# Kernel tuning notes

Measured on AMD Instinct MI355X. Metric: run time of the kernel, lower is better.

Reference implementation:

```python
import jax, jax.numpy as jnp
import numpy as np

INPUT_DIM = 512
HIDDEN_DIM = 1024
OUTPUT_DIM = 1000
BATCH = 256
SEQ_LEN = 256


def setup_inputs() -> dict:
    key = jax.random.key(0)
    ks = jax.random.split(key, 7)
    std = 1.0 / np.sqrt(HIDDEN_DIM)
    u = lambda k, shape: jax.random.uniform(k, shape, jnp.float32, -std, std)
    return {
        "x": jax.random.normal(ks[0], (BATCH, SEQ_LEN, INPUT_DIM), jnp.float32),
        "w_x2h": u(ks[1], (4 * HIDDEN_DIM, INPUT_DIM)),
        "b_x2h": u(ks[2], (4 * HIDDEN_DIM,)),
        "w_h2h": u(ks[3], (4 * HIDDEN_DIM, HIDDEN_DIM)),
        "b_h2h": u(ks[4], (4 * HIDDEN_DIM,)),
        "w_fc": u(ks[5], (OUTPUT_DIM, HIDDEN_DIM)),
        "b_fc": u(ks[6], (OUTPUT_DIM,)),
    }


def _lstm_last_hidden(x, w_x2h, b_x2h, w_h2h, b_h2h):
    B, T, D = x.shape
    H = w_h2h.shape[1]
    # Precompute input-to-hidden for all timesteps in one big GEMM: [B,T,4H]
    xg = jnp.einsum("btd,gd->btg", x, w_x2h) + b_x2h + b_h2h
    xg = jnp.swapaxes(xg, 0, 1)  # [T,B,4H] for scan

    def step(carry, xg_t):
        h, c = carry
        gates = xg_t + h @ w_h2h.T  # [B,4H]
        i, f, g, o = jnp.split(gates, 4, axis=1)
        i = jax.nn.sigmoid(i)
        f = jax.nn.sigmoid(f)
        g = jnp.tanh(g)
        o = jax.nn.sigmoid(o)
        c = c * f + i * g
        h = o * jnp.tanh(c)
        return (h, c), None

    h0 = jnp.zeros((B, H), x.dtype)
    c0 = jnp.zeros((B, H), x.dtype)
    (h_last, _), _ = jax.lax.scan(step, (h0, c0), xg)
    return h_last


def reference(x, w_x2h, b_x2h, w_h2h, b_h2h, w_fc, b_fc):
    h_last = _lstm_last_hidden(x, w_x2h, b_x2h, w_h2h, b_h2h)  # [B,H]
    return h_last @ w_fc.T + b_fc  # [B,OUTPUT_DIM]
```

## Files before the change

### kernel.cpp

```cpp
#include <hip/hip_runtime.h>

typedef __attribute__((ext_vector_type(8))) short short8;
typedef __attribute__((ext_vector_type(4))) float floatx4;

#define DIN  512
#define HSZ  1024
#define G4   4096
#define KTOT 1536
#define BQ   256
#define TT   256

#define MFMA __builtin_amdgcn_mfma_f32_16x16x32_bf16

__device__ __forceinline__ unsigned short f2bf(float f){
  unsigned int u = __float_as_uint(f);
  u += 0x7fffu + ((u >> 16) & 1u);
  return (unsigned short)(u >> 16);
}
__device__ __forceinline__ unsigned int pack2(float a, float b){
  return (unsigned int)f2bf(a) | ((unsigned int)f2bf(b) << 16);
}

__global__ void prep_wcat(const float* __restrict__ wx, const float* __restrict__ wh,
                          const float* __restrict__ bx, const float* __restrict__ bh,
                          unsigned short* __restrict__ Wcat, float* __restrict__ bias){
  int gid = blockIdx.x * blockDim.x + threadIdx.x;
  int idx = gid * 8;
  int g = idx / KTOT;
  int k = idx - g * KTOT;
  const float* src = (k < DIN) ? (wx + (size_t)g * DIN + k)
                               : (wh + (size_t)g * HSZ + (k - DIN));
  float4 f0 = *(const float4*)(src);
  float4 f1 = *(const float4*)(src + 4);
  uint4 v = make_uint4(pack2(f0.x,f0.y), pack2(f0.z,f0.w), pack2(f1.x,f1.y), pack2(f1.z,f1.w));
  *(uint4*)(Wcat + (size_t)g * KTOT + k) = v;
  if (gid < G4) bias[gid] = bx[gid] + bh[gid];
}

__global__ void prep_wfc(const float* __restrict__ wfc, unsigned short* __restrict__ Wfcb){
  int gid = blockIdx.x * blockDim.x + threadIdx.x;
  int idx = gid * 8;
  int n = idx >> 10;
  int k = idx & 1023;
  uint4 v;
  if (n < 1000){
    const float* src = wfc + (size_t)n * 1024 + k;
    float4 f0 = *(const float4*)(src);
    float4 f1 = *(const float4*)(src + 4);
    v = make_uint4(pack2(f0.x,f0.y), pack2(f0.z,f0.w), pack2(f1.x,f1.y), pack2(f1.z,f1.w));
  } else {
    v = make_uint4(0u, 0u, 0u, 0u);
  }
  *(uint4*)(Wfcb + idx) = v;
}

__global__ void prep_x(const float* __restrict__ x, unsigned short* __restrict__ xbf){
  int gid = blockIdx.x * 256 + threadIdx.x;
  int d8 = gid & 63;
  int b  = (gid >> 6) & 255;
  int t  = gid >> 14;
  const float* src = x + (((size_t)b * TT) + t) * DIN + d8 * 8;
  float4 f0 = *(const float4*)(src);
  float4 f1 = *(const float4*)(src + 4);
  uint4 v = make_uint4(pack2(f0.x,f0.y), pack2(f0.z,f0.w), pack2(f1.x,f1.y), pack2(f1.z,f1.w));
  *(uint4*)(xbf + (((size_t)t * BQ) + b) * DIN + d8 * 8) = v;
}

__global__ void init_misc(unsigned int* __restrict__ h0w, unsigned int* __restrict__ flags, int nflags){
  int gid = blockIdx.x * 256 + threadIdx.x;
  if (gid < 131072) h0w[gid] = 0u;
  if (gid < nflags) flags[gid] = 0u;
}

__global__ __launch_bounds__(512, 2)
void lstm_persist(const unsigned short* __restrict__ xbf,
                  const unsigned short* __restrict__ Wcat,
                  const float* __restrict__ bias,
                  unsigned short* __restrict__ hseq,
                  unsigned int* __restrict__ flags){
  extern __shared__ char smem[];
  char*  Ws  = smem;
  float* Gt2 = (float*)(smem + 98304);
  float* Bls = (float*)(smem + 98304 + 34816);
  __shared__ int mbx;

  const int tid  = threadIdx.x;
  const int bx   = blockIdx.x;
  const int bg   = bx >> 7;
  const int b0   = bg << 7;
  const int hb   = bx & 127;
  const int u0   = hb << 3;
  const int lane = tid & 63;
  const int w    = tid >> 6;
  const int kg   = w & 1;
  const int rg   = w >> 1;

  {
    int c  = tid >> 4;
    int ch = tid & 15;
    int grow = (c >> 3) * HSZ + u0 + (c & 7);
    const char* src = (const char*)(Wcat + (size_t)grow * KTOT);
    char* dst = Ws + c * 3072;
    int xr = (c & 7) << 4;
    #pragma unroll
    for (int q = 0; q < 12; ++q){
      int k2 = ch * 192 + q * 16;
      *(uint4*)(dst + (k2 ^ xr)) = *(const uint4*)(src + k2);
    }
    if (tid < 32) Bls[tid] = bias[(size_t)(tid >> 3) * HSZ + u0 + (tid & 7)];
    if (tid == 0) mbx = 0;
  }
  __syncthreads();

  const int kq8 = (lane >> 4) * 8;
  const int cA  = lane & 15;
  const int cB  = 16 + (lane & 15);
  const char* bpA = Ws + cA * 3072; const int xorA = (cA & 7) << 4;
  const char* bpB = Ws + cB * 3072; const int xorB = (cB & 7) << 4;

  const size_t rowA0 = (size_t)(b0 + rg * 32 + (lane & 15));

  const int er = tid >> 2;
  const int up = (tid & 3) * 2;
  float cst0 = 0.f, cst1 = 0.f;

  floatx4 xacc[2][2];

  auto compute_x = [&](int t){
    const unsigned short* xr0p = xbf + ((size_t)t * BQ + rowA0) * DIN + kg * 256 + kq8;
    const unsigned short* xr1p = xr0p + 16 * DIN;
    short8 X0[8], X1[8];
    #pragma unroll
    for (int p = 0; p < 8; ++p){
      X0[p] = *(const short8*)(xr0p + p * 32);
      X1[p] = *(const short8*)(xr1p + p * 32);
    }
    __builtin_amdgcn_sched_barrier(0);
    #pragma unroll
    for (int rf = 0; rf < 2; ++rf)
      #pragma unroll
      for (int cf = 0; cf < 2; ++cf)
        xacc[rf][cf] = (floatx4){0.f,0.f,0.f,0.f};
    const int bbase = kg * 512 + kq8 * 2;
    short8 bA[2], bB[2];
    bA[0] = *(const short8*)(bpA + ((bbase     ) ^ xorA));
    bB[0] = *(const short8*)(bpB + ((bbase     ) ^ xorB));
    bA[1] = *(const short8*)(bpA + ((bbase + 64) ^ xorA));
    bB[1] = *(const short8*)(bpB + ((bbase + 64) ^ xorB));
    #pragma unroll
    for (int j = 0; j < 8; ++j){
      const int sl = j & 1;
      short8 b0v = bA[sl], b1v = bB[sl];
      if (j < 6){
        int bb = bbase + (j + 2) * 64;
        bA[sl] = *(const short8*)(bpA + (bb ^ xorA));
        bB[sl] = *(const short8*)(bpB + (bb ^ xorB));
      }
      xacc[0][0] = MFMA(X0[j], b0v, xacc[0][0], 0, 0, 0);
      xacc[0][1] = MFMA(X0[j], b1v, xacc[0][1], 0, 0, 0);
      xacc[1][0] = MFMA(X1[j], b0v, xacc[1][0], 0, 0, 0);
      xacc[1][1] = MFMA(X1[j], b1v, xacc[1][1], 0, 0, 0);
    }
  };

  compute_x(0);

  const unsigned int* fz = flags + (bg << 7);

  for (int t = 0; t < TT; ++t){
    const unsigned short* hin  = hseq + (size_t)t * (BQ * HSZ);
    unsigned short*       hout = hseq + (size_t)(t + 1) * (BQ * HSZ);

    if (t > 0){
      if (w == 0){
        while (true){
          unsigned int va = __hip_atomic_load(fz + lane,      __ATOMIC_RELAXED, __HIP_MEMORY_SCOPE_AGENT);
          unsigned int vb = __hip_atomic_load(fz + 64 + lane, __ATOMIC_RELAXED, __HIP_MEMORY_SCOPE_AGENT);
          if (__ballot(va >= (unsigned)t && vb >= (unsigned)t) == ~0ull) break;
          __builtin_amdgcn_s_sleep(1);
        }
        if (lane == 0)
          __hip_atomic_store(&mbx, t, __ATOMIC_RELAXED, __HIP_MEMORY_SCOPE_WORKGROUP);
      } else {
        while (__hip_atomic_load(&mbx, __ATOMIC_RELAXED, __HIP_MEMORY_SCOPE_WORKGROUP) < t)
          __builtin_amdgcn_s_sleep(1);
      }
      asm volatile("" ::: "memory");
    }

    floatx4 hacc[2][2];
    #pragma unroll
    for (int rf = 0; rf < 2; ++rf)
      #pragma unroll
      for (int cf = 0; cf < 2; ++cf)
        hacc[rf][cf] = (floatx4){0.f,0.f,0.f,0.f};
    {
      const unsigned short* hr0 = hin + rowA0 * HSZ + kg * 512 + kq8;
      const unsigned short* hr1 = hr0 + 16 * HSZ;
      short8 HA0[16], HA1[16];
      #pragma unroll
      for (int p = 0; p < 16; ++p){
        HA0[p] = *(const short8*)(hr0 + p * 32);
        HA1[p] = *(const short8*)(hr1 + p * 32);
      }
      __builtin_amdgcn_sched_barrier(0);
      const int kb2 = 1024 + kg * 1024 + kq8 * 2;
      short8 bA[2], bB[2];
      bA[0] = *(const short8*)(bpA + ((kb2     ) ^ xorA));
      bB[0] = *(const short8*)(bpB + ((kb2     ) ^ xorB));
      bA[1] = *(const short8*)(bpA + ((kb2 + 64) ^ xorA));
      bB[1] = *(const short8*)(bpB + ((kb2 + 64) ^ xorB));
      #pragma unroll
      for (int j = 0; j < 16; ++j){
        const int sl = j & 1;
        short8 b0v = bA[sl], b1v = bB[sl];
        if (j < 14){
          int bb = kb2 + (j + 2) * 64;
          bA[sl] = *(const short8*)(bpA + (bb ^ xorA));
          bB[sl] = *(const short8*)(bpB + (bb ^ xorB));
        }
        hacc[0][0] = MFMA(HA0[j], b0v, hacc[0][0], 0, 0, 0);
        hacc[0][1] = MFMA(HA0[j], b1v, hacc[0][1], 0, 0, 0);
        hacc[1][0] = MFMA(HA1[j], b0v, hacc[1][0], 0, 0, 0);
        hacc[1][1] = MFMA(HA1[j], b1v, hacc[1][1], 0, 0, 0);
      }
    }

    {
      float* gdst = Gt2 + kg * (128 * 34);
      int r0 = rg * 32 + (lane >> 4) * 4;
      #pragma unroll
      for (int rf = 0; rf < 2; ++rf){
        floatx4 g0 = hacc[rf][0] + xacc[rf][0];
        floatx4 g1 = hacc[rf][1] + xacc[rf][1];
        #pragma unroll
        for (int r = 0; r < 4; ++r){
          gdst[(r0 + rf * 16 + r) * 34 + cA] = g0[r];
          gdst[(r0 + rf * 16 + r) * 34 + cB] = g1[r];
        }
      }
    }
    __syncthreads();

    {
      const float* g0p = Gt2 + er * 34;
      const float* g1p = g0p + 128 * 34;
      float gi0 = g0p[     up] + g1p[     up] + Bls[     up];
      float gf0 = g0p[ 8 + up] + g1p[ 8 + up] + Bls[ 8 + up];
      float gg0 = g0p[16 + up] + g1p[16 + up] + Bls[16 + up];
      float go0 = g0p[24 + up] + g1p[24 + up] + Bls[24 + up];
      float gi1 = g0p[     up + 1] + g1p[     up + 1] + Bls[     up + 1];
      float gf1 = g0p[ 8 + up + 1] + g1p[ 8 + up + 1] + Bls[ 8 + up + 1];
      float gg1 = g0p[16 + up + 1] + g1p[16 + up + 1] + Bls[16 + up + 1];
      float go1 = g0p[24 + up + 1] + g1p[24 + up + 1] + Bls[24 + up + 1];

      float iv0 = 1.f / (1.f + __expf(-gi0));
      float fv0 = 1.f / (1.f + __expf(-gf0));
      float e20 = __expf(-2.f * fmaxf(fminf(gg0, 30.f), -30.f));
      float gv0 = (1.f - e20) / (1.f + e20);
      float ov0 = 1.f / (1.f + __expf(-go0));
      float cn0 = cst0 * fv0 + iv0 * gv0;
      cst0 = cn0;
      float ec0 = __expf(-2.f * fmaxf(fminf(cn0, 30.f), -30.f));
      float hv0 = ov0 * (1.f - ec0) / (1.f + ec0);

      float iv1 = 1.f / (1.f + __expf(-gi1));
      float fv1 = 1.f / (1.f + __expf(-gf1));
      float e21 = __expf(-2.f * fmaxf(fminf(gg1, 30.f), -30.f));
      float gv1 = (1.f - e21) / (1.f + e21);
      float ov1 = 1.f / (1.f + __expf(-go1));
      float cn1 = cst1 * fv1 + iv1 * gv1;
      cst1 = cn1;
      float ec1 = __expf(-2.f * fmaxf(fminf(cn1, 30.f), -30.f));
      float hv1 = ov1 * (1.f - ec1) / (1.f + ec1);

      __hip_atomic_store((unsigned int*)(hout + (size_t)(b0 + er) * HSZ + u0 + up),
                         pack2(hv0, hv1), __ATOMIC_RELAXED, __HIP_MEMORY_SCOPE_AGENT);
    }
    __syncthreads();

    if (tid == 0)
      __hip_atomic_store((unsigned int*)(fz + hb), (unsigned)(t + 1),
                         __ATOMIC_RELAXED, __HIP_MEMORY_SCOPE_AGENT);

    if (t + 1 < TT) compute_x(t + 1);
  }
}

__global__ __launch_bounds__(256, 1)
void fc_kernel(const unsigned short* __restrict__ h, const unsigned short* __restrict__ wfc,
               const float* __restrict__ bfc, float* __restrict__ out){
  int bx = blockIdx.x, tid = threadIdx.x;
  int wave = tid >> 6, lane = tid & 63;
  int row0 = (bx >> 4) * 64 + wave * 16;
  int col0 = (bx & 15) * 64;
  int lr = lane & 15, lk = (lane >> 4) * 8;
  floatx4 acc[4] = {{0.f,0.f,0.f,0.f},{0.f,0.f,0.f,0.f},{0.f,0.f,0.f,0.f},{0.f,0.f,0.f,0.f}};
  #pragma unroll 4
  for (int ks = 0; ks < 32; ++ks){
    int k = ks * 32 + lk;
    short8 a = *(const short8*)(h + (size_t)(row0 + lr) * 1024 + k);
    #pragma unroll
    for (int fj = 0; fj < 4; ++fj){
      short8 b = *(const short8*)(wfc + (size_t)(col0 + fj * 16 + lr) * 1024 + k);
      acc[fj] = MFMA(a, b, acc[fj], 0, 0, 0);
    }
  }
  #pragma unroll
  for (int fj = 0; fj < 4; ++fj){
    int col = col0 + fj * 16 + lr;
    if (col < 1000){
      #pragma unroll
      for (int r = 0; r < 4; ++r){
        int row = row0 + (lane >> 4) * 4 + r;
        out[(size_t)row * 1000 + col] = acc[fj][r] + bfc[col];
      }
    }
  }
}

extern "C" void kernel_launch(void* const* d_in, const int* in_sizes, int n_in,
                              void* d_out, int out_size, void* d_ws, size_t ws_size,
                              hipStream_t stream){
  const float* x    = (const float*)d_in[0];
  const float* wx2h = (const float*)d_in[1];
  const float* bx2h = (const float*)d_in[2];
  const float* wh2h = (const float*)d_in[3];
  const float* bh2h = (const float*)d_in[4];
  const float* wfc  = (const float*)d_in[5];
  const float* bfc  = (const float*)d_in[6];
  float* out = (float*)d_out;
  char* ws = (char*)d_ws;

  unsigned short* Wcat  = (unsigned short*)(ws + 0);
  unsigned short* Wfcb  = (unsigned short*)(ws + 12582912);
  float*          bias  = (float*)         (ws + 14680064);
  unsigned short* xbf   = (unsigned short*)(ws + 14696448);
  unsigned short* hseq  = (unsigned short*)(ws + 81805312);
  unsigned int*   flags = (unsigned int*)  (ws + 216547328);

  (void)hipFuncSetAttribute((const void*)lstm_persist,
                            hipFuncAttributeMaxDynamicSharedMemorySize, 133376);

  hipLaunchKernelGGL(prep_wcat, dim3(3072), dim3(256), 0, stream, wx2h, wh2h, bx2h, bh2h, Wcat, bias);
  hipLaunchKernelGGL(prep_wfc,  dim3(512),  dim3(256), 0, stream, wfc, Wfcb);
  hipLaunchKernelGGL(prep_x,    dim3(16384),dim3(256), 0, stream, x, xbf);
  hipLaunchKernelGGL(init_misc, dim3(512),  dim3(256), 0, stream,
                     (unsigned int*)hseq, flags, 256);

  hipLaunchKernelGGL(lstm_persist, dim3(256), dim3(512), 133376, stream,
                     xbf, Wcat, bias, hseq, flags);

  hipLaunchKernelGGL(fc_kernel, dim3(64), dim3(256), 0, stream,
                     hseq + (size_t)256 * BQ * HSZ, Wfcb, bfc, out);
}
```

Measured before the change: 3.775 ms.

## Interleave two batch-half recurrence chains per block, each block owning four hidden units

Each persistent block now owns 4 hidden units across the full batch instead of 8 units for half the batch. The block alternates between the two batch-half chains every timestep, so each chain's flag wait (256 producers) overlaps with work on the other chain. It also halves the per-block weight slice in LDS, and the inline x-projection now runs after the flag wait is issued instead of being precomputed. The risks are wider barriers over 256 flags, half the threads idle in the elementwise phase, and lower MFMA work per wave.

```diff
diff --git a/kernel.cpp b/kernel.cpp
--- a/kernel.cpp
+++ b/kernel.cpp
@@ -80,120 +80,101 @@
                   unsigned int* __restrict__ flags){
   extern __shared__ char smem[];
   char*  Ws  = smem;
-  float* Gt2 = (float*)(smem + 98304);
-  float* Bls = (float*)(smem + 98304 + 34816);
-  __shared__ int mbx;
+  float* Gt2 = (float*)(smem + 49152);
+  float* Bls = (float*)(smem + 67584);
 
   const int tid  = threadIdx.x;
   const int bx   = blockIdx.x;
-  const int bg   = bx >> 7;
-  const int b0   = bg << 7;
-  const int hb   = bx & 127;
-  const int u0   = hb << 3;
+  const int u0   = bx << 2;
   const int lane = tid & 63;
   const int w    = tid >> 6;
   const int kg   = w & 1;
   const int rg   = w >> 1;
 
   {
-    int c  = tid >> 4;
-    int ch = tid & 15;
-    int grow = (c >> 3) * HSZ + u0 + (c & 7);
+    int c   = tid >> 5;
+    int chn = tid & 31;
+    int grow = (c >> 2) * HSZ + u0 + (c & 3);
     const char* src = (const char*)(Wcat + (size_t)grow * KTOT);
     char* dst = Ws + c * 3072;
     int xr = (c & 7) << 4;
     #pragma unroll
-    for (int q = 0; q < 12; ++q){
-      int k2 = ch * 192 + q * 16;
+    for (int q = 0; q < 6; ++q){
+      int k2 = chn * 96 + q * 16;
       *(uint4*)(dst + (k2 ^ xr)) = *(const uint4*)(src + k2);
     }
-    if (tid < 32) Bls[tid] = bias[(size_t)(tid >> 3) * HSZ + u0 + (tid & 7)];
-    if (tid == 0) mbx = 0;
+    if (tid < 16) Bls[tid] = bias[(size_t)(tid >> 2) * HSZ + u0 + (tid & 3)];
   }
   __syncthreads();
 
   const int kq8 = (lane >> 4) * 8;
   const int cA  = lane & 15;
-  const int cB  = 16 + (lane & 15);
-  const char* bpA = Ws + cA * 3072; const int xorA = (cA & 7) << 4;
-  const char* bpB = Ws + cB * 3072; const int xorB = (cB & 7) << 4;
-
-  const size_t rowA0 = (size_t)(b0 + rg * 32 + (lane & 15));
-
-  const int er = tid >> 2;
-  const int up = (tid & 3) * 2;
-  float cst0 = 0.f, cst1 = 0.f;
-
-  floatx4 xacc[2][2];
-
-  auto compute_x = [&](int t){
-    const unsigned short* xr0p = xbf + ((size_t)t * BQ + rowA0) * DIN + kg * 256 + kq8;
-    const unsigned short* xr1p = xr0p + 16 * DIN;
-    short8 X0[8], X1[8];
-    #pragma unroll
-    for (int p = 0; p < 8; ++p){
-      X0[p] = *(const short8*)(xr0p + p * 32);
-      X1[p] = *(const short8*)(xr1p + p * 32);
-    }
-    __builtin_amdgcn_sched_barrier(0);
-    #pragma unroll
-    for (int rf = 0; rf < 2; ++rf)
-      #pragma unroll
-      for (int cf = 0; cf < 2; ++cf)
-        xacc[rf][cf] = (floatx4){0.f,0.f,0.f,0.f};
-    const int bbase = kg * 512 + kq8 * 2;
-    short8 bA[2], bB[2];
-    bA[0] = *(const short8*)(bpA + ((bbase     ) ^ xorA));
-    bB[0] = *(const short8*)(bpB + ((bbase     ) ^ xorB));
-    bA[1] = *(const short8*)(bpA + ((bbase + 64) ^ xorA));
-    bB[1] = *(const short8*)(bpB + ((bbase + 64) ^ xorB));
-    #pragma unroll
-    for (int j = 0; j < 8; ++j){
-      const int sl = j & 1;
-      short8 b0v = bA[sl], b1v = bB[sl];
-      if (j < 6){
-        int bb = bbase + (j + 2) * 64;
-        bA[sl] = *(const short8*)(bpA + (bb ^ xorA));
-        bB[sl] = *(const short8*)(bpB + (bb ^ xorB));
-      }
-      xacc[0][0] = MFMA(X0[j], b0v, xacc[0][0], 0, 0, 0);
-      xacc[0][1] = MFMA(X0[j], b1v, xacc[0][1], 0, 0, 0);
-      xacc[1][0] = MFMA(X1[j], b0v, xacc[1][0], 0, 0, 0);
-      xacc[1][1] = MFMA(X1[j], b1v, xacc[1][1], 0, 0, 0);
-    }
-  };
-
-  compute_x(0);
-
-  const unsigned int* fz = flags + (bg << 7);
-
-  for (int t = 0; t < TT; ++t){
+  const char* bpA = Ws + cA * 3072;
+  const int xorA = (cA & 7) << 4;
+
+  const int erow = tid >> 1;
+  const int eup  = (tid & 1) * 2;
+
+  float cA0 = 0.f, cA1 = 0.f;
+  float cB0 = 0.f, cB1 = 0.f;
+
+  auto step_chain = [&](int chain, int t, float& cs0, float& cs1){
     const unsigned short* hin  = hseq + (size_t)t * (BQ * HSZ);
     unsigned short*       hout = hseq + (size_t)(t + 1) * (BQ * HSZ);
+    const size_t rowA0 = (size_t)(chain * 128 + rg * 32 + (lane & 15));
+
+    short8 X0[8], X1[8];
+    {
+      const unsigned short* xr0p = xbf + ((size_t)t * BQ + rowA0) * DIN + kg * 256 + kq8;
+      const unsigned short* xr1p = xr0p + 16 * DIN;
+      #pragma unroll
+      for (int p = 0; p < 8; ++p){
+        X0[p] = *(const short8*)(xr0p + p * 32);
+        X1[p] = *(const short8*)(xr1p + p * 32);
+      }
+    }
+    __builtin_amdgcn_sched_barrier(0);
 
     if (t > 0){
-      if (w == 0){
+      if (tid < 64){
+        const unsigned int* fz = flags + (chain << 8);
         while (true){
-          unsigned int va = __hip_atomic_load(fz + lane,      __ATOMIC_RELAXED, __HIP_MEMORY_SCOPE_AGENT);
-          unsigned int vb = __hip_atomic_load(fz + 64 + lane, __ATOMIC_RELAXED, __HIP_MEMORY_SCOPE_AGENT);
-          if (__ballot(va >= (unsigned)t && vb >= (unsigned)t) == ~0ull) break;
-          __builtin_amdgcn_s_sleep(1);
+          unsigned int v0 = __hip_atomic_load(fz + lane,       __ATOMIC_RELAXED, __HIP_MEMORY_SCOPE_AGENT);
+          unsigned int v1 = __hip_atomic_load(fz + 64  + lane, __ATOMIC_RELAXED, __HIP_MEMORY_SCOPE_AGENT);
+          unsigned int v2 = __hip_atomic_load(fz + 128 + lane, __ATOMIC_RELAXED, __HIP_MEMORY_SCOPE_AGENT);
+          unsigned int v3 = __hip_atomic_load(fz + 192 + lane, __ATOMIC_RELAXED, __HIP_MEMORY_SCOPE_AGENT);
+          bool ok = (v0 >= (unsigned)t) && (v1 >= (unsigned)t) &&
+                    (v2 >= (unsigned)t) && (v3 >= (unsigned)t);
+          if (__ballot(ok) == ~0ull) break;
+          __builtin_amdgcn_s_sleep(2);
         }
-        if (lane == 0)
-          __hip_atomic_store(&mbx, t, __ATOMIC_RELAXED, __HIP_MEMORY_SCOPE_WORKGROUP);
-      } else {
-        while (__hip_atomic_load(&mbx, __ATOMIC_RELAXED, __HIP_MEMORY_SCOPE_WORKGROUP) < t)
-          __builtin_amdgcn_s_sleep(1);
-      }
+      }
+      __syncthreads();
       asm volatile("" ::: "memory");
     }
 
-    floatx4 hacc[2][2];
+    floatx4 acc[2][2];
     #pragma unroll
-    for (int rf = 0; rf < 2; ++rf)
-      #pragma unroll
-      for (int cf = 0; cf < 2; ++cf)
-        hacc[rf][cf] = (floatx4){0.f,0.f,0.f,0.f};
+    for (int ab = 0; ab < 2; ++ab)
+      #pragma unroll
+      for (int rf = 0; rf < 2; ++rf)
+        acc[ab][rf] = (floatx4){0.f,0.f,0.f,0.f};
+
+    {
+      const int bbase = kg * 512 + kq8 * 2;
+      short8 bA[2];
+      bA[0] = *(const short8*)(bpA + ((bbase     ) ^ xorA));
+      bA[1] = *(const short8*)(bpA + ((bbase + 64) ^ xorA));
+      #pragma unroll
+      for (int j = 0; j < 8; ++j){
+        const int sl = j & 1;
+        short8 b0v = bA[sl];
+        if (j < 6) bA[sl] = *(const short8*)(bpA + ((bbase + (j + 2) * 64) ^ xorA));
+        acc[sl][0] = MFMA(X0[j], b0v, acc[sl][0], 0, 0, 0);
+        acc[sl][1] = MFMA(X1[j], b0v, acc[sl][1], 0, 0, 0);
+      }
+    }
+
     {
       const unsigned short* hr0 = hin + rowA0 * HSZ + kg * 512 + kq8;
       const unsigned short* hr1 = hr0 + 16 * HSZ;
@@ -205,62 +186,51 @@
       }
       __builtin_amdgcn_sched_barrier(0);
       const int kb2 = 1024 + kg * 1024 + kq8 * 2;
-      short8 bA[2], bB[2];
+      short8 bA[2];
       bA[0] = *(const short8*)(bpA + ((kb2     ) ^ xorA));
-      bB[0] = *(const short8*)(bpB + ((kb2     ) ^ xorB));
       bA[1] = *(const short8*)(bpA + ((kb2 + 64) ^ xorA));
-      bB[1] = *(const short8*)(bpB + ((kb2 + 64) ^ xorB));
       #pragma unroll
       for (int j = 0; j < 16; ++j){
         const int sl = j & 1;
-        short8 b0v = bA[sl], b1v = bB[sl];
-        if (j < 14){
-          int bb = kb2 + (j + 2) * 64;
-          bA[sl] = *(const short8*)(bpA + (bb ^ xorA));
-          bB[sl] = *(const short8*)(bpB + (bb ^ xorB));
-        }
-        hacc[0][0] = MFMA(HA0[j], b0v, hacc[0][0], 0, 0, 0);
-        hacc[0][1] = MFMA(HA0[j], b1v, hacc[0][1], 0, 0, 0);
-        hacc[1][0] = MFMA(HA1[j], b0v, hacc[1][0], 0, 0, 0);
-        hacc[1][1] = MFMA(HA1[j], b1v, hacc[1][1], 0, 0, 0);
+        short8 b0v = bA[sl];
+        if (j < 14) bA[sl] = *(const short8*)(bpA + ((kb2 + (j + 2) * 64) ^ xorA));
+        acc[sl][0] = MFMA(HA0[j], b0v, acc[sl][0], 0, 0, 0);
+        acc[sl][1] = MFMA(HA1[j], b0v, acc[sl][1], 0, 0, 0);
       }
     }
 
     {
-      float* gdst = Gt2 + kg * (128 * 34);
+      float* gd = Gt2 + kg * (128 * 18);
       int r0 = rg * 32 + (lane >> 4) * 4;
       #pragma unroll
       for (int rf = 0; rf < 2; ++rf){
-        floatx4 g0 = hacc[rf][0] + xacc[rf][0];
-        floatx4 g1 = hacc[rf][1] + xacc[rf][1];
+        floatx4 g = acc[0][rf] + acc[1][rf];
         #pragma unroll
-        for (int r = 0; r < 4; ++r){
-          gdst[(r0 + rf * 16 + r) * 34 + cA] = g0[r];
-          gdst[(r0 + rf * 16 + r) * 34 + cB] = g1[r];
-        }
+        for (int r = 0; r < 4; ++r)
+          gd[(r0 + rf * 16 + r) * 18 + cA] = g[r];
       }
     }
     __syncthreads();
 
-    {
-      const float* g0p = Gt2 + er * 34;
-      const float* g1p = g0p + 128 * 34;
-      float gi0 = g0p[     up] + g1p[     up] + Bls[     up];
-      float gf0 = g0p[ 8 + up] + g1p[ 8 + up] + Bls[ 8 + up];
-      float gg0 = g0p[16 + up] + g1p[16 + up] + Bls[16 + up];
-      float go0 = g0p[24 + up] + g1p[24 + up] + Bls[24 + up];
-      float gi1 = g0p[     up + 1] + g1p[     up + 1] + Bls[     up + 1];
-      float gf1 = g0p[ 8 + up + 1] + g1p[ 8 + up + 1] + Bls[ 8 + up + 1];
-      float gg1 = g0p[16 + up + 1] + g1p[16 + up + 1] + Bls[16 + up + 1];
-      float go1 = g0p[24 + up + 1] + g1p[24 + up + 1] + Bls[24 + up + 1];
+    if (tid < 256){
+      const float* g0p = Gt2 + erow * 18;
+      const float* g1p = g0p + 128 * 18;
+      float gi0 = g0p[     eup] + g1p[     eup] + Bls[     eup];
+      float gf0 = g0p[ 4 + eup] + g1p[ 4 + eup] + Bls[ 4 + eup];
+      float gg0 = g0p[ 8 + eup] + g1p[ 8 + eup] + Bls[ 8 + eup];
+      float go0 = g0p[12 + eup] + g1p[12 + eup] + Bls[12 + eup];
+      float gi1 = g0p[     eup + 1] + g1p[     eup + 1] + Bls[     eup + 1];
+      float gf1 = g0p[ 4 + eup + 1] + g1p[ 4 + eup + 1] + Bls[ 4 + eup + 1];
+      float gg1 = g0p[ 8 + eup + 1] + g1p[ 8 + eup + 1] + Bls[ 8 + eup + 1];
+      float go1 = g0p[12 + eup + 1] + g1p[12 + eup + 1] + Bls[12 + eup + 1];
 
       float iv0 = 1.f / (1.f + __expf(-gi0));
       float fv0 = 1.f / (1.f + __expf(-gf0));
       float e20 = __expf(-2.f * fmaxf(fminf(gg0, 30.f), -30.f));
       float gv0 = (1.f - e20) / (1.f + e20);
       float ov0 = 1.f / (1.f + __expf(-go0));
-      float cn0 = cst0 * fv0 + iv0 * gv0;
-      cst0 = cn0;
+      float cn0 = cs0 * fv0 + iv0 * gv0;
+      cs0 = cn0;
       float ec0 = __expf(-2.f * fmaxf(fminf(cn0, 30.f), -30.f));
       float hv0 = ov0 * (1.f - ec0) / (1.f + ec0);
 
@@ -269,21 +239,24 @@
       float e21 = __expf(-2.f * fmaxf(fminf(gg1, 30.f), -30.f));
       float gv1 = (1.f - e21) / (1.f + e21);
       float ov1 = 1.f / (1.f + __expf(-go1));
-      float cn1 = cst1 * fv1 + iv1 * gv1;
-      cst1 = cn1;
+      float cn1 = cs1 * fv1 + iv1 * gv1;
+      cs1 = cn1;
       float ec1 = __expf(-2.f * fmaxf(fminf(cn1, 30.f), -30.f));
       float hv1 = ov1 * (1.f - ec1) / (1.f + ec1);
 
-      __hip_atomic_store((unsigned int*)(hout + (size_t)(b0 + er) * HSZ + u0 + up),
+      __hip_atomic_store((unsigned int*)(hout + (size_t)(chain * 128 + erow) * HSZ + u0 + eup),
                          pack2(hv0, hv1), __ATOMIC_RELAXED, __HIP_MEMORY_SCOPE_AGENT);
     }
     __syncthreads();
 
     if (tid == 0)
-      __hip_atomic_store((unsigned int*)(fz + hb), (unsigned)(t + 1),
+      __hip_atomic_store(&flags[(chain << 8) + bx], (unsigned)(t + 1),
                          __ATOMIC_RELAXED, __HIP_MEMORY_SCOPE_AGENT);
-
-    if (t + 1 < TT) compute_x(t + 1);
+  };
+
+  for (int t = 0; t < TT; ++t){
+    step_chain(0, t, cA0, cA1);
+    step_chain(1, t, cB0, cB1);
   }
 }
 
@@ -340,15 +313,15 @@
   unsigned int*   flags = (unsigned int*)  (ws + 216547328);
 
   (void)hipFuncSetAttribute((const void*)lstm_persist,
-                            hipFuncAttributeMaxDynamicSharedMemorySize, 133376);
+                            hipFuncAttributeMaxDynamicSharedMemorySize, 67712);
 
   hipLaunchKernelGGL(prep_wcat, dim3(3072), dim3(256), 0, stream, wx2h, wh2h, bx2h, bh2h, Wcat, bias);
   hipLaunchKernelGGL(prep_wfc,  dim3(512),  dim3(256), 0, stream, wfc, Wfcb);
   hipLaunchKernelGGL(prep_x,    dim3(16384),dim3(256), 0, stream, x, xbf);
   hipLaunchKernelGGL(init_misc, dim3(512),  dim3(256), 0, stream,
-                     (unsigned int*)hseq, flags, 256);
-
-  hipLaunchKernelGGL(lstm_persist, dim3(256), dim3(512), 133376, stream,
+                     (unsigned int*)hseq, flags, 512);
+
+  hipLaunchKernelGGL(lstm_persist, dim3(256), dim3(512), 67712, stream,
                      xbf, Wcat, bias, hseq, flags);
 
   hipLaunchKernelGGL(fc_kernel, dim3(64), dim3(256), 0, stream,
```

Measured after the change: 6.007 ms. +59.1%, slower.

## Replace persistent LSTM kernel with per-timestep launches and ping-pong hidden buffers

Applied to the files above, without the earlier changes.

Drops the persistent kernel and its inter-block flag spin-waits. It now launches one lstm_step kernel per timestep, swapping between two hidden buffers and keeping the cell state in global memory instead of registers. Each launch reloads its weight slice into shared memory, and the x-projection is no longer overlapped with the wait for the previous step. This removes the cost of atomic flag polling, but adds 256 kernel launches, a weight reload per step and a global read/write of the cell state every step.

```diff
diff --git a/kernel.cpp b/kernel.cpp
--- a/kernel.cpp
+++ b/kernel.cpp
@@ -66,23 +66,23 @@
   *(uint4*)(xbf + (((size_t)t * BQ) + b) * DIN + d8 * 8) = v;
 }
 
-__global__ void init_misc(unsigned int* __restrict__ h0w, unsigned int* __restrict__ flags, int nflags){
+__global__ void init_misc(unsigned int* __restrict__ h0w, unsigned int* __restrict__ cw){
   int gid = blockIdx.x * 256 + threadIdx.x;
   if (gid < 131072) h0w[gid] = 0u;
-  if (gid < nflags) flags[gid] = 0u;
+  cw[gid] = 0u;
 }
 
 __global__ __launch_bounds__(512, 2)
-void lstm_persist(const unsigned short* __restrict__ xbf,
-                  const unsigned short* __restrict__ Wcat,
-                  const float* __restrict__ bias,
-                  unsigned short* __restrict__ hseq,
-                  unsigned int* __restrict__ flags){
+void lstm_step(const unsigned short* __restrict__ xt,
+               const unsigned short* __restrict__ Wcat,
+               const float* __restrict__ bias,
+               const unsigned short* __restrict__ hin,
+               unsigned short* __restrict__ hout,
+               float* __restrict__ cstg){
   extern __shared__ char smem[];
   char*  Ws  = smem;
   float* Gt2 = (float*)(smem + 98304);
   float* Bls = (float*)(smem + 98304 + 34816);
-  __shared__ int mbx;
 
   const int tid  = threadIdx.x;
   const int bx   = blockIdx.x;
@@ -95,6 +95,21 @@
   const int kg   = w & 1;
   const int rg   = w >> 1;
 
+  const int kq8 = (lane >> 4) * 8;
+  const size_t rowA0 = (size_t)(b0 + rg * 32 + (lane & 15));
+
+  short8 X0[8], X1[8];
+  {
+    const unsigned short* xr0p = xt + rowA0 * DIN + kg * 256 + kq8;
+    const unsigned short* xr1p = xr0p + 16 * DIN;
+    #pragma unroll
+    for (int p = 0; p < 8; ++p){
+      X0[p] = *(const short8*)(xr0p + p * 32);
+      X1[p] = *(const short8*)(xr1p + p * 32);
+    }
+  }
+  __builtin_amdgcn_sched_barrier(0);
+
   {
     int c  = tid >> 4;
     int ch = tid & 15;
@@ -108,39 +123,24 @@
       *(uint4*)(dst + (k2 ^ xr)) = *(const uint4*)(src + k2);
     }
     if (tid < 32) Bls[tid] = bias[(size_t)(tid >> 3) * HSZ + u0 + (tid & 7)];
-    if (tid == 0) mbx = 0;
   }
   __syncthreads();
 
-  const int kq8 = (lane >> 4) * 8;
   const int cA  = lane & 15;
   const int cB  = 16 + (lane & 15);
   const char* bpA = Ws + cA * 3072; const int xorA = (cA & 7) << 4;
   const char* bpB = Ws + cB * 3072; const int xorB = (cB & 7) << 4;
 
-  const size_t rowA0 = (size_t)(b0 + rg * 32 + (lane & 15));
-
-  const int er = tid >> 2;
-  const int up = (tid & 3) * 2;
-  float cst0 = 0.f, cst1 = 0.f;
-
-  floatx4 xacc[2][2];
-
-  auto compute_x = [&](int t){
-    const unsigned short* xr0p = xbf + ((size_t)t * BQ + rowA0) * DIN + kg * 256 + kq8;
-    const unsigned short* xr1p = xr0p + 16 * DIN;
-    short8 X0[8], X1[8];
-    #pragma unroll
-    for (int p = 0; p < 8; ++p){
-      X0[p] = *(const short8*)(xr0p + p * 32);
-      X1[p] = *(const short8*)(xr1p + p * 32);
-    }
-    __builtin_amdgcn_sched_barrier(0);
+  floatx4 acc[2][2][2];
+  #pragma unroll
+  for (int ab = 0; ab < 2; ++ab)
     #pragma unroll
     for (int rf = 0; rf < 2; ++rf)
       #pragma unroll
       for (int cf = 0; cf < 2; ++cf)
-        xacc[rf][cf] = (floatx4){0.f,0.f,0.f,0.f};
+        acc[ab][rf][cf] = (floatx4){0.f,0.f,0.f,0.f};
+
+  {
     const int bbase = kg * 512 + kq8 * 2;
     short8 bA[2], bB[2];
     bA[0] = *(const short8*)(bpA + ((bbase     ) ^ xorA));
@@ -156,134 +156,98 @@
         bA[sl] = *(const short8*)(bpA + (bb ^ xorA));
         bB[sl] = *(const short8*)(bpB + (bb ^ xorB));
       }
-      xacc[0][0] = MFMA(X0[j], b0v, xacc[0][0], 0, 0, 0);
-      xacc[0][1] = MFMA(X0[j], b1v, xacc[0][1], 0, 0, 0);
-      xacc[1][0] = MFMA(X1[j], b0v, xacc[1][0], 0, 0, 0);
-      xacc[1][1] = MFMA(X1[j], b1v, xacc[1][1], 0, 0, 0);
-    }
-  };
-
-  compute_x(0);
-
-  const unsigned int* fz = flags + (bg << 7);
-
-  for (int t = 0; t < TT; ++t){
-    const unsigned short* hin  = hseq + (size_t)t * (BQ * HSZ);
-    unsigned short*       hout = hseq + (size_t)(t + 1) * (BQ * HSZ);
-
-    if (t > 0){
-      if (w == 0){
-        while (true){
-          unsigned int va = __hip_atomic_load(fz + lane,      __ATOMIC_RELAXED, __HIP_MEMORY_SCOPE_AGENT);
-          unsigned int vb = __hip_atomic_load(fz + 64 + lane, __ATOMIC_RELAXED, __HIP_MEMORY_SCOPE_AGENT);
-          if (__ballot(va >= (unsigned)t && vb >= (unsigned)t) == ~0ull) break;
-          __builtin_amdgcn_s_sleep(1);
-        }
-        if (lane == 0)
-          __hip_atomic_store(&mbx, t, __ATOMIC_RELAXED, __HIP_MEMORY_SCOPE_WORKGROUP);
-      } else {
-        while (__hip_atomic_load(&mbx, __ATOMIC_RELAXED, __HIP_MEMORY_SCOPE_WORKGROUP) < t)
-          __builtin_amdgcn_s_sleep(1);
+      acc[sl][0][0] = MFMA(X0[j], b0v, acc[sl][0][0], 0, 0, 0);
+      acc[sl][0][1] = MFMA(X0[j], b1v, acc[sl][0][1], 0, 0, 0);
+      acc[sl][1][0] = MFMA(X1[j], b0v, acc[sl][1][0], 0, 0, 0);
+      acc[sl][1][1] = MFMA(X1[j], b1v, acc[sl][1][1], 0, 0, 0);
+    }
+  }
+
+  {
+    const unsigned short* hr0 = hin + rowA0 * HSZ + kg * 512 + kq8;
+    const unsigned short* hr1 = hr0 + 16 * HSZ;
+    short8 HA0[16], HA1[16];
+    #pragma unroll
+    for (int p = 0; p < 16; ++p){
+      HA0[p] = *(const short8*)(hr0 + p * 32);
+      HA1[p] = *(const short8*)(hr1 + p * 32);
+    }
+    __builtin_amdgcn_sched_barrier(0);
+    const int kb2 = 1024 + kg * 1024 + kq8 * 2;
+    short8 bA[2], bB[2];
+    bA[0] = *(const short8*)(bpA + ((kb2     ) ^ xorA));
+    bB[0] = *(const short8*)(bpB + ((kb2     ) ^ xorB));
+    bA[1] = *(const short8*)(bpA + ((kb2 + 64) ^ xorA));
+    bB[1] = *(const short8*)(bpB + ((kb2 + 64) ^ xorB));
+    #pragma unroll
+    for (int j = 0; j < 16; ++j){
+      const int sl = j & 1;
+      short8 b0v = bA[sl], b1v = bB[sl];
+      if (j < 14){
+        int bb = kb2 + (j + 2) * 64;
+        bA[sl] = *(const short8*)(bpA + (bb ^ xorA));
+        bB[sl] = *(const short8*)(bpB + (bb ^ xorB));
       }
-      asm volatile("" ::: "memory");
-    }
-
-    floatx4 hacc[2][2];
-    #pragma unroll
-    for (int rf = 0; rf < 2; ++rf)
+      acc[sl][0][0] = MFMA(HA0[j], b0v, acc[sl][0][0], 0, 0, 0);
+      acc[sl][0][1] = MFMA(HA0[j], b1v, acc[sl][0][1], 0, 0, 0);
+      acc[sl][1][0] = MFMA(HA1[j], b0v, acc[sl][1][0], 0, 0, 0);
+      acc[sl][1][1] = MFMA(HA1[j], b1v, acc[sl][1][1], 0, 0, 0);
+    }
+  }
+
+  {
+    float* gdst = Gt2 + kg * (128 * 34);
+    int r0 = rg * 32 + (lane >> 4) * 4;
+    #pragma unroll
+    for (int rf = 0; rf < 2; ++rf){
+      floatx4 g0 = acc[0][rf][0] + acc[1][rf][0];
+      floatx4 g1 = acc[0][rf][1] + acc[1][rf][1];
       #pragma unroll
-      for (int cf = 0; cf < 2; ++cf)
-        hacc[rf][cf] = (floatx4){0.f,0.f,0.f,0.f};
-    {
-      const unsigned short* hr0 = hin + rowA0 * HSZ + kg * 512 + kq8;
-      const unsigned short* hr1 = hr0 + 16 * HSZ;
-      short8 HA0[16], HA1[16];
-      #pragma unroll
-      for (int p = 0; p < 16; ++p){
-        HA0[p] = *(const short8*)(hr0 + p * 32);
-        HA1[p] = *(const short8*)(hr1 + p * 32);
+      for (int r = 0; r < 4; ++r){
+        gdst[(r0 + rf * 16 + r) * 34 + cA] = g0[r];
+        gdst[(r0 + rf * 16 + r) * 34 + cB] = g1[r];
       }
-      __builtin_amdgcn_sched_barrier(0);
-      const int kb2 = 1024 + kg * 1024 + kq8 * 2;
-      short8 bA[2], bB[2];
-      bA[0] = *(const short8*)(bpA + ((kb2     ) ^ xorA));
-      bB[0] = *(const short8*)(bpB + ((kb2     ) ^ xorB));
-      bA[1] = *(const short8*)(bpA + ((kb2 + 64) ^ xorA));
-      bB[1] = *(const short8*)(bpB + ((kb2 + 64) ^ xorB));
-      #pragma unroll
-      for (int j = 0; j < 16; ++j){
-        const int sl = j & 1;
-        short8 b0v = bA[sl], b1v = bB[sl];
-        if (j < 14){
-          int bb = kb2 + (j + 2) * 64;
-          bA[sl] = *(const short8*)(bpA + (bb ^ xorA));
-          bB[sl] = *(const short8*)(bpB + (bb ^ xorB));
-        }
-        hacc[0][0] = MFMA(HA0[j], b0v, hacc[0][0], 0, 0, 0);
-        hacc[0][1] = MFMA(HA0[j], b1v, hacc[0][1], 0, 0, 0);
-        hacc[1][0] = MFMA(HA1[j], b0v, hacc[1][0], 0, 0, 0);
-        hacc[1][1] = MFMA(HA1[j], b1v, hacc[1][1], 0, 0, 0);
-      }
-    }
-
-    {
-      float* gdst = Gt2 + kg * (128 * 34);
-      int r0 = rg * 32 + (lane >> 4) * 4;
-      #pragma unroll
-      for (int rf = 0; rf < 2; ++rf){
-        floatx4 g0 = hacc[rf][0] + xacc[rf][0];
-        floatx4 g1 = hacc[rf][1] + xacc[rf][1];
-        #pragma unroll
-        for (int r = 0; r < 4; ++r){
-          gdst[(r0 + rf * 16 + r) * 34 + cA] = g0[r];
-          gdst[(r0 + rf * 16 + r) * 34 + cB] = g1[r];
-        }
-      }
-    }
-    __syncthreads();
-
-    {
-      const float* g0p = Gt2 + er * 34;
-      const float* g1p = g0p + 128 * 34;
-      float gi0 = g0p[     up] + g1p[     up] + Bls[     up];
-      float gf0 = g0p[ 8 + up] + g1p[ 8 + up] + Bls[ 8 + up];
-      float gg0 = g0p[16 + up] + g1p[16 + up] + Bls[16 + up];
-      float go0 = g0p[24 + up] + g1p[24 + up] + Bls[24 + up];
-      float gi1 = g0p[     up + 1] + g1p[     up + 1] + Bls[     up + 1];
-      float gf1 = g0p[ 8 + up + 1] + g1p[ 8 + up + 1] + Bls[ 8 + up + 1];
-      float gg1 = g0p[16 + up + 1] + g1p[16 + up + 1] + Bls[16 + up + 1];
-      float go1 = g0p[24 + up + 1] + g1p[24 + up + 1] + Bls[24 + up + 1];
-
-      float iv0 = 1.f / (1.f + __expf(-gi0));
-      float fv0 = 1.f / (1.f + __expf(-gf0));
-      float e20 = __expf(-2.f * fmaxf(fminf(gg0, 30.f), -30.f));
-      float gv0 = (1.f - e20) / (1.f + e20);
-      float ov0 = 1.f / (1.f + __expf(-go0));
-      float cn0 = cst0 * fv0 + iv0 * gv0;
-      cst0 = cn0;
-      float ec0 = __expf(-2.f * fmaxf(fminf(cn0, 30.f), -30.f));
-      float hv0 = ov0 * (1.f - ec0) / (1.f + ec0);
-
-      float iv1 = 1.f / (1.f + __expf(-gi1));
-      float fv1 = 1.f / (1.f + __expf(-gf1));
-      float e21 = __expf(-2.f * fmaxf(fminf(gg1, 30.f), -30.f));
-      float gv1 = (1.f - e21) / (1.f + e21);
-      float ov1 = 1.f / (1.f + __expf(-go1));
-      float cn1 = cst1 * fv1 + iv1 * gv1;
-      cst1 = cn1;
-      float ec1 = __expf(-2.f * fmaxf(fminf(cn1, 30.f), -30.f));
-      float hv1 = ov1 * (1.f - ec1) / (1.f + ec1);
-
-      __hip_atomic_store((unsigned int*)(hout + (size_t)(b0 + er) * HSZ + u0 + up),
-                         pack2(hv0, hv1), __ATOMIC_RELAXED, __HIP_MEMORY_SCOPE_AGENT);
-    }
-    __syncthreads();
-
-    if (tid == 0)
-      __hip_atomic_store((unsigned int*)(fz + hb), (unsigned)(t + 1),
-                         __ATOMIC_RELAXED, __HIP_MEMORY_SCOPE_AGENT);
-
-    if (t + 1 < TT) compute_x(t + 1);
+    }
+  }
+  __syncthreads();
+
+  {
+    const int er = tid >> 2;
+    const int up = (tid & 3) * 2;
+    const float* g0p = Gt2 + er * 34;
+    const float* g1p = g0p + 128 * 34;
+    float gi0 = g0p[     up] + g1p[     up] + Bls[     up];
+    float gf0 = g0p[ 8 + up] + g1p[ 8 + up] + Bls[ 8 + up];
+    float gg0 = g0p[16 + up] + g1p[16 + up] + Bls[16 + up];
+    float go0 = g0p[24 + up] + g1p[24 + up] + Bls[24 + up];
+    float gi1 = g0p[     up + 1] + g1p[     up + 1] + Bls[     up + 1];
+    float gf1 = g0p[ 8 + up + 1] + g1p[ 8 + up + 1] + Bls[ 8 + up + 1];
+    float gg1 = g0p[16 + up + 1] + g1p[16 + up + 1] + Bls[16 + up + 1];
+    float go1 = g0p[24 + up + 1] + g1p[24 + up + 1] + Bls[24 + up + 1];
+
+    float2* cp = (float2*)(cstg + (size_t)(b0 + er) * HSZ + u0 + up);
+    float2 cv = *cp;
+
+    float iv0 = 1.f / (1.f + __expf(-gi0));
+    float fv0 = 1.f / (1.f + __expf(-gf0));
+    float e20 = __expf(-2.f * fmaxf(fminf(gg0, 30.f), -30.f));
+    float gv0 = (1.f - e20) / (1.f + e20);
+    float ov0 = 1.f / (1.f + __expf(-go0));
+    float cn0 = cv.x * fv0 + iv0 * gv0;
+    float ec0 = __expf(-2.f * fmaxf(fminf(cn0, 30.f), -30.f));
+    float hv0 = ov0 * (1.f - ec0) / (1.f + ec0);
+
+    float iv1 = 1.f / (1.f + __expf(-gi1));
+    float fv1 = 1.f / (1.f + __expf(-gf1));
+    float e21 = __expf(-2.f * fmaxf(fminf(gg1, 30.f), -30.f));
+    float gv1 = (1.f - e21) / (1.f + e21);
+    float ov1 = 1.f / (1.f + __expf(-go1));
+    float cn1 = cv.y * fv1 + iv1 * gv1;
+    float ec1 = __expf(-2.f * fmaxf(fminf(cn1, 30.f), -30.f));
+    float hv1 = ov1 * (1.f - ec1) / (1.f + ec1);
+
+    *cp = make_float2(cn0, cn1);
+    *(unsigned int*)(hout + (size_t)(b0 + er) * HSZ + u0 + up) = pack2(hv0, hv1);
   }
 }
 
@@ -332,25 +296,28 @@
   float* out = (float*)d_out;
   char* ws = (char*)d_ws;
 
-  unsigned short* Wcat  = (unsigned short*)(ws + 0);
-  unsigned short* Wfcb  = (unsigned short*)(ws + 12582912);
-  float*          bias  = (float*)         (ws + 14680064);
-  unsigned short* xbf   = (unsigned short*)(ws + 14696448);
-  unsigned short* hseq  = (unsigned short*)(ws + 81805312);
-  unsigned int*   flags = (unsigned int*)  (ws + 216547328);
-
-  (void)hipFuncSetAttribute((const void*)lstm_persist,
+  unsigned short* Wcat = (unsigned short*)(ws + 0);
+  unsigned short* Wfcb = (unsigned short*)(ws + 12582912);
+  float*          bias = (float*)         (ws + 14680064);
+  unsigned short* xbf  = (unsigned short*)(ws + 14696448);
+  unsigned short* h0   = (unsigned short*)(ws + 81805312);
+  unsigned short* h1   = (unsigned short*)(ws + 82329600);
+  float*          cstg = (float*)         (ws + 82853888);
+
+  (void)hipFuncSetAttribute((const void*)lstm_step,
                             hipFuncAttributeMaxDynamicSharedMemorySize, 133376);
 
   hipLaunchKernelGGL(prep_wcat, dim3(3072), dim3(256), 0, stream, wx2h, wh2h, bx2h, bh2h, Wcat, bias);
   hipLaunchKernelGGL(prep_wfc,  dim3(512),  dim3(256), 0, stream, wfc, Wfcb);
   hipLaunchKernelGGL(prep_x,    dim3(16384),dim3(256), 0, stream, x, xbf);
-  hipLaunchKernelGGL(init_misc, dim3(512),  dim3(256), 0, stream,
-                     (unsigned int*)hseq, flags, 256);
-
-  hipLaunchKernelGGL(lstm_persist, dim3(256), dim3(512), 133376, stream,
-                     xbf, Wcat, bias, hseq, flags);
-
-  hipLaunchKernelGGL(fc_kernel, dim3(64), dim3(256), 0, stream,
-                     hseq + (size_t)256 * BQ * HSZ, Wfcb, bfc, out);
-}
+  hipLaunchKernelGGL(init_misc, dim3(1024), dim3(256), 0, stream,
+                     (unsigned int*)h0, (unsigned int*)cstg);
+
+  for (int t = 0; t < TT; ++t){
+    const unsigned short* hin = (t & 1) ? h1 : h0;
+    unsigned short*      hout = (t & 1) ? h0 : h1;
+    hipLaunchKernelGGL(lstm_step, dim3(256), dim3(512), 133376, stream,
+                       xbf + (size_t)t * BQ * DIN, Wcat, bias, hin, hout, cstg);
+  }
+  hipLaunchKernelGGL(fc_kernel, dim3(64), dim3(256), 0, stream, h0, Wfcb, bfc, out);
+}
```

Measured after the change: 4.540 ms. +20.2%, slower.
